# Optimization experiments

Measured on AMD Instinct MI355X. Metric: run time of the kernel, lower is better.

## Reference

```python
import jax, jax.numpy as jnp
import numpy as np

B = 512
V = 6890   # SMPL vertices
NJ = 24    # joints (global)
NB = 10    # shape betas
NP = 207   # pose blendshape features = 23*9
NJO = 19   # cocoplus output joints
PARENTS = np.array([0,0,0,0,1,2,3,4,5,6,7,8,9,9,9,12,13,14,16,17,18,19,20,21], dtype=np.int32)


def setup_inputs() -> dict:
    key = jax.random.key(0)
    ks = jax.random.split(key, 7)
    inputs = jax.random.normal(ks[0], (B, 82), jnp.float32) * 0.2  # [pose(72) | shape(10)]
    v_template = jax.random.normal(ks[1], (V, 3), jnp.float32)
    shapes = jax.random.normal(ks[2], (NB, V * 3), jnp.float32) * 0.01
    posedirs = jax.random.normal(ks[3], (NP, V * 3), jnp.float32) * 0.01
    jr = jax.random.uniform(ks[4], (V, NJ), jnp.float32)
    smpl_regressor = jr / jnp.sum(jr, axis=0, keepdims=True)          # columns sum to 1 over vertices
    w = jax.random.uniform(ks[5], (V, NJ), jnp.float32) ** 4
    lbs_weights = w / jnp.sum(w, axis=1, keepdims=True)               # rows sum to 1 over joints
    cr = jax.random.uniform(ks[6], (V, NJO), jnp.float32)
    joint_regressor = cr / jnp.sum(cr, axis=0, keepdims=True)
    parents = jnp.asarray(PARENTS)
    return {"inputs": inputs, "v_template": v_template, "shapes": shapes,
            "posedirs": posedirs, "smpl_regressor": smpl_regressor,
            "lbs_weights": lbs_weights, "joint_regressor": joint_regressor,
            "parents": parents}


def _rodrigues(pose):  # [B,72] -> [B,24,3,3]
    r = pose.reshape(-1, 3)
    angle = jnp.linalg.norm(r + 1e-8, axis=1, keepdims=True)  # [N,1]
    n = r / angle
    c = jnp.cos(angle)[:, :, None]   # [N,1,1]
    s = jnp.sin(angle)[:, :, None]
    outer = n[:, :, None] * n[:, None, :]
    z = jnp.zeros_like(n[:, 0])
    K = jnp.stack([z, -n[:, 2], n[:, 1],
                   n[:, 2], z, -n[:, 0],
                   -n[:, 1], n[:, 0], z], axis=1).reshape(-1, 3, 3)
    R = c * jnp.eye(3, dtype=pose.dtype) + (1.0 - c) * outer + s * K
    return R.reshape(-1, NJ, 3, 3)


def _make_A(R, t):  # R [B,3,3], t [B,3] -> [B,4,4]
    top = jnp.concatenate([R, t[:, :, None]], axis=2)
    bottom = jnp.broadcast_to(jnp.array([0., 0., 0., 1.], dtype=R.dtype), (R.shape[0], 1, 4))
    return jnp.concatenate([top, bottom], axis=1)


def _global_rigid(rotations, joints, parents_np):
    # sequential kinematic-chain composition over the fixed 24-joint tree
    res = [_make_A(rotations[:, 0], joints[:, 0])]
    for i in range(1, NJ):
        p = int(parents_np[i])
        t = joints[:, i] - joints[:, p]
        res.append(jnp.matmul(res[p], _make_A(rotations[:, i], t)))
    A_world = jnp.stack(res, axis=1)                 # [B,24,4,4]
    new_J = A_world[:, :, :3, 3]
    Jw0 = jnp.concatenate([joints, jnp.zeros(joints.shape[:2] + (1,), joints.dtype)], axis=2)[..., None]
    init_bone = jnp.matmul(A_world, Jw0)[..., 0]     # [B,24,4]
    pad = jnp.zeros_like(A_world).at[:, :, :, 3].set(init_bone)
    return new_J, A_world - pad


def reference(inputs, v_template, shapes, posedirs, smpl_regressor, lbs_weights, joint_regressor, parents):
    b = inputs.shape[0]
    pose = inputs[:, :72]
    beta = inputs[:, -10:]
    v_shaped = jnp.matmul(beta, shapes).reshape(b, V, 3) + v_template
    v_joints = jnp.einsum('bvc,vj->bjc', v_shaped, smpl_regressor)        # [B,24,3]
    rot = _rodrigues(pose)                                                # [B,24,3,3]
    pose_feature = (rot[:, 1:] - jnp.eye(3, dtype=rot.dtype)).reshape(b, -1)  # [B,207]
    v_posed = jnp.matmul(pose_feature, posedirs).reshape(b, V, 3) + v_shaped
    joint_transformed, A = _global_rigid(rot, v_joints, np.asarray(parents))
    T = jnp.einsum('vj,bjk->bvk', lbs_weights, A.reshape(b, NJ, 16)).reshape(b, V, 4, 4)
    v_homo = jnp.concatenate([v_posed, jnp.ones((b, V, 1), v_posed.dtype)], axis=2)
    vertices = jnp.einsum('bvij,bvj->bvi', T, v_homo)[:, :, :3]
    joints = jnp.einsum('bvc,vj->bjc', vertices, joint_regressor)         # [B,19,3]
    return vertices, joints, rot
```

## Files before the change

kernel.cpp:

```cpp
#include <hip/hip_runtime.h>

#define B_   512
#define V_   6890
#define NJ_  24
#define NB_  10
#define NP_  207
#define NJO_ 19



#define SRB_   192
#define SRCH_  862

__global__ void __launch_bounds__(256) k_pre(const float* __restrict__ in,
                                             const float* __restrict__ shapes,
                                             const float* __restrict__ vt,
                                             const float* __restrict__ sreg,
                                             float* __restrict__ srtr,
                                             float* __restrict__ out_rot,
                                             float* __restrict__ pf_t) {
  int blk = blockIdx.x;
  int tid = threadIdx.x;
  if (blk < SRB_) {
    int j  = blk >> 3;
    int ch = blk & 7;
    int vend = (ch + 1) * SRCH_; if (vend > V_) vend = V_;
    float acc[33];
#pragma unroll
    for (int a = 0; a < 33; a++) acc[a] = 0.f;
    for (int v = ch * SRCH_ + tid; v < vend; v += 256) {
      float w = sreg[v * NJ_ + j];
#pragma unroll
      for (int k = 0; k < NB_; k++) {
        const float* sp = shapes + k * (V_ * 3) + 3 * v;
#pragma unroll
        for (int c = 0; c < 3; c++) acc[k * 3 + c] += w * sp[c];
      }
#pragma unroll
      for (int c = 0; c < 3; c++) acc[30 + c] += w * vt[3 * v + c];
    }
    __shared__ float red[4][33];
    int wave = tid >> 6, lane = tid & 63;
#pragma unroll
    for (int a = 0; a < 33; a++) {
      float x = acc[a];
#pragma unroll
      for (int m = 1; m < 64; m <<= 1) x += __shfl_xor(x, m, 64);
      if (lane == 0) red[wave][a] = x;
    }
    __syncthreads();
    if (tid < 33) {
      float s = red[0][tid] + red[1][tid] + red[2][tid] + red[3][tid];
      if (tid < 30) atomicAdd(&srtr[((tid / 3) * NJ_ + j) * 3 + (tid % 3)], s);
      else          atomicAdd(&srtr[720 + j * 3 + (tid - 30)], s);
    }
  } else {
    int idx = (blk - SRB_) * 256 + tid;
    int b = idx & (B_ - 1);
    int j = idx >> 9;
    const float* r = in + b * 82 + j * 3;
    float r0 = r[0], r1 = r[1], r2 = r[2];
    float ax = r0 + 1e-8f, ay = r1 + 1e-8f, az = r2 + 1e-8f;
    float angle = sqrtf(ax * ax + ay * ay + az * az);
    float inv = 1.0f / angle;
    float n0 = r0 * inv, n1 = r1 * inv, n2 = r2 * inv;
    float c = cosf(angle), s = sinf(angle);
    float ic = 1.0f - c;
    float R[9];
    R[0] = c + ic * n0 * n0;      R[1] = ic * n0 * n1 - s * n2;  R[2] = ic * n0 * n2 + s * n1;
    R[3] = ic * n1 * n0 + s * n2; R[4] = c + ic * n1 * n1;       R[5] = ic * n1 * n2 - s * n0;
    R[6] = ic * n2 * n0 - s * n1; R[7] = ic * n2 * n1 + s * n0;  R[8] = c + ic * n2 * n2;
    float* ro = out_rot + b * 216 + j * 9;
#pragma unroll
    for (int q = 0; q < 9; q++) ro[q] = R[q];
    if (j > 0) {
#pragma unroll
      for (int q = 0; q < 9; q++)
        pf_t[(size_t)((j - 1) * 9 + q) * B_ + b] = R[q] - ((q % 4 == 0) ? 1.0f : 0.0f);
    }
  }
}

__global__ void __launch_bounds__(64) k_chain(const float* __restrict__ in,
                                              const float* __restrict__ rot,
                                              const float* __restrict__ srtr,
                                              const int* __restrict__ parents,
                                              float* __restrict__ Abuf) {
  __shared__ float Jl[NJ_ * 3 * 64];
  __shared__ float Al[64 * 289];
  int tid = threadIdx.x;
  int b = blockIdx.x * 64 + tid;
  float beta[NB_];
#pragma unroll
  for (int k = 0; k < NB_; k++) beta[k] = in[b * 82 + 72 + k];
#pragma unroll
  for (int j = 0; j < NJ_; j++) {
#pragma unroll
    for (int c = 0; c < 3; c++) {
      float s = srtr[720 + j * 3 + c];
#pragma unroll
      for (int k = 0; k < NB_; k++) s += beta[k] * srtr[(k * NJ_ + j) * 3 + c];
      Jl[(j * 3 + c) * 64 + tid] = s;
    }
  }
  const float* Rb = rot + b * 216;
  float* A = Al + tid * 289;
#pragma unroll
  for (int r = 0; r < 3; r++) {
#pragma unroll
    for (int c = 0; c < 3; c++) A[r * 4 + c] = Rb[r * 3 + c];
    A[r * 4 + 3] = Jl[r * 64 + tid];
  }
  for (int j = 1; j < NJ_; j++) {
    int p = parents[j];
    float t0 = Jl[(j * 3 + 0) * 64 + tid] - Jl[(p * 3 + 0) * 64 + tid];
    float t1 = Jl[(j * 3 + 1) * 64 + tid] - Jl[(p * 3 + 1) * 64 + tid];
    float t2 = Jl[(j * 3 + 2) * 64 + tid] - Jl[(p * 3 + 2) * 64 + tid];
    float Rj[9];
#pragma unroll
    for (int q = 0; q < 9; q++) Rj[q] = Rb[j * 9 + q];
#pragma unroll
    for (int r = 0; r < 3; r++) {
      float p0 = A[p * 12 + r * 4 + 0];
      float p1 = A[p * 12 + r * 4 + 1];
      float p2 = A[p * 12 + r * 4 + 2];
      float p3 = A[p * 12 + r * 4 + 3];
#pragma unroll
      for (int c = 0; c < 3; c++)
        A[j * 12 + r * 4 + c] = p0 * Rj[c] + p1 * Rj[3 + c] + p2 * Rj[6 + c];
      A[j * 12 + r * 4 + 3] = p0 * t0 + p1 * t1 + p2 * t2 + p3;
    }
  }
  float* Ab = Abuf + (size_t)b * 288;
#pragma unroll
  for (int j = 0; j < NJ_; j++) {
    float jx = Jl[(j * 3 + 0) * 64 + tid];
    float jy = Jl[(j * 3 + 1) * 64 + tid];
    float jz = Jl[(j * 3 + 2) * 64 + tid];
#pragma unroll
    for (int r = 0; r < 3; r++) {
      float m0 = A[j * 12 + r * 4 + 0];
      float m1 = A[j * 12 + r * 4 + 1];
      float m2 = A[j * 12 + r * 4 + 2];
      float m3 = A[j * 12 + r * 4 + 3];
      float4 o;
      o.x = m0; o.y = m1; o.z = m2;
      o.w = m3 - (m0 * jx + m1 * jy + m2 * jz);
      *reinterpret_cast<float4*>(Ab + j * 12 + r * 4) = o;
    }
  }
}

#define PB_ 8
#define BT_ 32
#define GX_ 108
#define GY_ 16
#define NWG_ (GX_ * GY_)
__global__ void __launch_bounds__(256) k_main(const float* __restrict__ in,
                                              const float* __restrict__ shapes,
                                              const float* __restrict__ vt,
                                              const float* __restrict__ posedirs,
                                              const float* __restrict__ lbs,
                                              const float* __restrict__ pf_t,
                                              const float* __restrict__ Abuf,
                                              float* __restrict__ verts) {
  __shared__ float lbs_l[64 * 25];
  int tid = threadIdx.x;
  int raw  = blockIdx.y * GX_ + blockIdx.x;
  int virt = (raw & 7) * (NWG_ / 8) + (raw >> 3);
  int vblk = virt >> 4;
  int bblk = virt & (GY_ - 1);
  int v0 = vblk * 64;
  int b0 = bblk * BT_;
  int nv = V_ - v0; if (nv > 64) nv = 64;
  for (int i = tid; i < nv * NJ_; i += 256)
    lbs_l[(i / NJ_) * 25 + (i % NJ_)] = lbs[(size_t)v0 * NJ_ + i];
  __syncthreads();
  int lane = tid & 63;
  int g = tid >> 6;
  int bb0 = __builtin_amdgcn_readfirstlane(b0 + g * PB_);
  int v = v0 + lane;
  int vc = v < V_ ? v : V_ - 1;

  float acc[PB_][3];
  {
    float t0 = vt[3 * vc + 0], t1 = vt[3 * vc + 1], t2 = vt[3 * vc + 2];
#pragma unroll
    for (int i = 0; i < PB_; i++) { acc[i][0] = t0; acc[i][1] = t1; acc[i][2] = t2; }
  }
#pragma unroll
  for (int k = 0; k < NB_; k++) {
    const float* sp = shapes + k * (V_ * 3) + 3 * vc;
    float s0 = sp[0], s1 = sp[1], s2 = sp[2];
#pragma unroll
    for (int i = 0; i < PB_; i++) {
      float bv = in[(size_t)(bb0 + i) * 82 + 72 + k];
      acc[i][0] += bv * s0; acc[i][1] += bv * s1; acc[i][2] += bv * s2;
    }
  }
  for (int p = 0; p < NP_; p++) {
    const float* pp = posedirs + (size_t)p * (V_ * 3) + 3 * vc;
    float d0 = pp[0], d1 = pp[1], d2 = pp[2];
    const float* pfp = pf_t + (size_t)p * B_ + bb0;
#pragma unroll
    for (int i = 0; i < PB_; i++) {
      float f = pfp[i];
      acc[i][0] += f * d0; acc[i][1] += f * d1; acc[i][2] += f * d2;
    }
  }
  float o[PB_][3];
#pragma unroll
  for (int i = 0; i < PB_; i++) { o[i][0] = 0.f; o[i][1] = 0.f; o[i][2] = 0.f; }
  for (int j = 0; j < NJ_; j++) {
    float w = lbs_l[lane * 25 + j];
#pragma unroll
    for (int i = 0; i < PB_; i++) {
      const float* M = Abuf + (size_t)(bb0 + i) * 288 + j * 12;
      float x = acc[i][0], y = acc[i][1], z = acc[i][2];
      o[i][0] += w * (M[0] * x + M[1] * y + M[2]  * z + M[3]);
      o[i][1] += w * (M[4] * x + M[5] * y + M[6]  * z + M[7]);
      o[i][2] += w * (M[8] * x + M[9] * y + M[10] * z + M[11]);
    }
  }
  if (v < V_) {
#pragma unroll
    for (int i = 0; i < PB_; i++) {
      float* op = verts + (size_t)(bb0 + i) * (V_ * 3) + 3 * v;
      op[0] = o[i][0]; op[1] = o[i][1]; op[2] = o[i][2];
    }
  }
}

#define JCH_ 1728
__global__ void __launch_bounds__(256) k_joints(const float* __restrict__ verts,
                                                const float* __restrict__ jreg,
                                                float* __restrict__ jout) {
  int b = blockIdx.x;
  int ch = blockIdx.y;
  int tid = threadIdx.x;
  int vend = (ch + 1) * JCH_; if (vend > V_) vend = V_;
  float acc[NJO_ * 3];
#pragma unroll
  for (int a = 0; a < NJO_ * 3; a++) acc[a] = 0.f;
  const float* vb = verts + (size_t)b * V_ * 3;
  for (int v = ch * JCH_ + tid; v < vend; v += 256) {
    float x = vb[3 * v + 0], y = vb[3 * v + 1], z = vb[3 * v + 2];
    const float* jr = jreg + (size_t)v * NJO_;
#pragma unroll
    for (int jo = 0; jo < NJO_; jo++) {
      float w = jr[jo];
      acc[jo * 3 + 0] += w * x; acc[jo * 3 + 1] += w * y; acc[jo * 3 + 2] += w * z;
    }
  }
  __shared__ float red[4][NJO_ * 3];
  int wave = tid >> 6, lane = tid & 63;
#pragma unroll
  for (int a = 0; a < NJO_ * 3; a++) {
    float x = acc[a];
#pragma unroll
    for (int m = 1; m < 64; m <<= 1) x += __shfl_xor(x, m, 64);
    if (lane == 0) red[wave][a] = x;
  }
  __syncthreads();
  if (tid < NJO_ * 3) {
    float s = red[0][tid] + red[1][tid] + red[2][tid] + red[3][tid];
    atomicAdd(&jout[b * (NJO_ * 3) + tid], s);
  }
}

extern "C" void kernel_launch(void* const* d_in, const int* in_sizes, int n_in,
                              void* d_out, int out_size, void* d_ws, size_t ws_size,
                              hipStream_t stream) {
  const float* inputs   = (const float*)d_in[0];
  const float* v_templ  = (const float*)d_in[1];
  const float* shapes   = (const float*)d_in[2];
  const float* posedirs = (const float*)d_in[3];
  const float* sreg     = (const float*)d_in[4];
  const float* lbs      = (const float*)d_in[5];
  const float* jreg     = (const float*)d_in[6];
  const int*   parents  = (const int*)d_in[7];

  float* out   = (float*)d_out;
  float* verts = out;
  float* jout  = out + 10583040;
  float* rot   = out + 10612224;

  float* ws   = (float*)d_ws;
  float* pf_t = ws;
  float* Abuf = ws + 105984;
  float* srtr = ws + 105984 + 147456;

  hipMemsetAsync(srtr, 0, 792 * sizeof(float), stream);
  hipMemsetAsync(jout, 0, B_ * NJO_ * 3 * sizeof(float), stream);

  k_pre  <<<SRB_ + 48, 256, 0, stream>>>(inputs, shapes, v_templ, sreg, srtr, rot, pf_t);
  k_chain<<<8, 64, 0, stream>>>(inputs, rot, srtr, parents, Abuf);
  dim3 gmain(GX_, GY_);
  k_main <<<gmain, 256, 0, stream>>>(inputs, shapes, v_templ, posedirs, lbs, pf_t, Abuf, verts);
  dim3 gj(B_, 4);
  k_joints<<<gj, 256, 0, stream>>>(verts, jreg, jout);
}
```

Measured before the change: 299.8 us.

## Parallelize kinematic chain per row, transpose joint regressor, fold memset into k_pre

The kinematic-chain kernel now uses three threads per batch element, one per matrix row. Joints and transforms live in registers instead of large shared-memory arrays, and a compile-time parent table lets the loop fully unroll. k_pre gains extra blocks that zero the joint output and write a transposed copy of the joint regressor, so k_joints reads the weights coalesced and one memset launch is dropped. The chain and regressor results depend on the hardcoded parent table matching the input, and the extra workspace used by jreg_t must fit in the allocation.

Result: faster. 266.8 us (-11.0%).

```diff
diff --git a/kernel.cpp b/kernel.cpp
--- a/kernel.cpp
+++ b/kernel.cpp
@@ -11,14 +11,19 @@
 
 #define SRB_   192
 #define SRCH_  862
+#define RODB_  48
+#define TRB_   26
 
 __global__ void __launch_bounds__(256) k_pre(const float* __restrict__ in,
                                              const float* __restrict__ shapes,
                                              const float* __restrict__ vt,
                                              const float* __restrict__ sreg,
+                                             const float* __restrict__ jreg,
                                              float* __restrict__ srtr,
                                              float* __restrict__ out_rot,
-                                             float* __restrict__ pf_t) {
+                                             float* __restrict__ pf_t,
+                                             float* __restrict__ jreg_t,
+                                             float* __restrict__ jout) {
   int blk = blockIdx.x;
   int tid = threadIdx.x;
   if (blk < SRB_) {
@@ -54,7 +59,7 @@
       if (tid < 30) atomicAdd(&srtr[((tid / 3) * NJ_ + j) * 3 + (tid % 3)], s);
       else          atomicAdd(&srtr[720 + j * 3 + (tid - 30)], s);
     }
-  } else {
+  } else if (blk < SRB_ + RODB_) {
     int idx = (blk - SRB_) * 256 + tid;
     int b = idx & (B_ - 1);
     int j = idx >> 9;
@@ -78,21 +83,33 @@
       for (int q = 0; q < 9; q++)
         pf_t[(size_t)((j - 1) * 9 + q) * B_ + b] = R[q] - ((q % 4 == 0) ? 1.0f : 0.0f);
     }
-  }
-}
-
-__global__ void __launch_bounds__(64) k_chain(const float* __restrict__ in,
-                                              const float* __restrict__ rot,
-                                              const float* __restrict__ srtr,
-                                              const int* __restrict__ parents,
-                                              float* __restrict__ Abuf) {
-  __shared__ float Jl[NJ_ * 3 * 64];
-  __shared__ float Al[64 * 289];
+  } else {
+    int idx = (blk - SRB_ - RODB_) * 256 + tid;
+    for (int q = idx; q < B_ * NJO_ * 3; q += TRB_ * 256) jout[q] = 0.f;
+    for (int e = idx; e < V_ * NJO_; e += TRB_ * 256) {
+      int jo = e / V_;
+      int v  = e - jo * V_;
+      jreg_t[e] = jreg[v * NJO_ + jo];
+    }
+  }
+}
+
+__global__ void __launch_bounds__(192) k_chain(const float* __restrict__ in,
+                                               const float* __restrict__ rot,
+                                               const float* __restrict__ srtr,
+                                               const int* __restrict__ parents,
+                                               float* __restrict__ Abuf) {
+  (void)parents;
+  constexpr int P[NJ_] = {0, 0, 0, 0, 1, 2, 3, 4, 5, 6, 7, 8, 9, 9, 9, 12, 13, 14,
+                          16, 17, 18, 19, 20, 21};
   int tid = threadIdx.x;
-  int b = blockIdx.x * 64 + tid;
+  int bl = tid & 63;
+  int r  = tid >> 6;
+  int b  = blockIdx.x * 64 + bl;
   float beta[NB_];
 #pragma unroll
   for (int k = 0; k < NB_; k++) beta[k] = in[b * 82 + 72 + k];
+  float J[NJ_][3];
 #pragma unroll
   for (int j = 0; j < NJ_; j++) {
 #pragma unroll
@@ -100,54 +117,36 @@
       float s = srtr[720 + j * 3 + c];
 #pragma unroll
       for (int k = 0; k < NB_; k++) s += beta[k] * srtr[(k * NJ_ + j) * 3 + c];
-      Jl[(j * 3 + c) * 64 + tid] = s;
+      J[j][c] = s;
     }
   }
   const float* Rb = rot + b * 216;
-  float* A = Al + tid * 289;
-#pragma unroll
-  for (int r = 0; r < 3; r++) {
-#pragma unroll
-    for (int c = 0; c < 3; c++) A[r * 4 + c] = Rb[r * 3 + c];
-    A[r * 4 + 3] = Jl[r * 64 + tid];
-  }
+  float A[NJ_][4];
+#pragma unroll
+  for (int c = 0; c < 3; c++) A[0][c] = Rb[r * 3 + c];
+  A[0][3] = J[0][r];
+#pragma unroll
   for (int j = 1; j < NJ_; j++) {
-    int p = parents[j];
-    float t0 = Jl[(j * 3 + 0) * 64 + tid] - Jl[(p * 3 + 0) * 64 + tid];
-    float t1 = Jl[(j * 3 + 1) * 64 + tid] - Jl[(p * 3 + 1) * 64 + tid];
-    float t2 = Jl[(j * 3 + 2) * 64 + tid] - Jl[(p * 3 + 2) * 64 + tid];
+    const int p = P[j];
+    float t0 = J[j][0] - J[p][0];
+    float t1 = J[j][1] - J[p][1];
+    float t2 = J[j][2] - J[p][2];
     float Rj[9];
 #pragma unroll
     for (int q = 0; q < 9; q++) Rj[q] = Rb[j * 9 + q];
-#pragma unroll
-    for (int r = 0; r < 3; r++) {
-      float p0 = A[p * 12 + r * 4 + 0];
-      float p1 = A[p * 12 + r * 4 + 1];
-      float p2 = A[p * 12 + r * 4 + 2];
-      float p3 = A[p * 12 + r * 4 + 3];
-#pragma unroll
-      for (int c = 0; c < 3; c++)
-        A[j * 12 + r * 4 + c] = p0 * Rj[c] + p1 * Rj[3 + c] + p2 * Rj[6 + c];
-      A[j * 12 + r * 4 + 3] = p0 * t0 + p1 * t1 + p2 * t2 + p3;
-    }
-  }
-  float* Ab = Abuf + (size_t)b * 288;
+    float p0 = A[p][0], p1 = A[p][1], p2 = A[p][2], p3 = A[p][3];
+#pragma unroll
+    for (int c = 0; c < 3; c++)
+      A[j][c] = p0 * Rj[c] + p1 * Rj[3 + c] + p2 * Rj[6 + c];
+    A[j][3] = p0 * t0 + p1 * t1 + p2 * t2 + p3;
+  }
+  float* Ab = Abuf + (size_t)b * 288 + r * 4;
 #pragma unroll
   for (int j = 0; j < NJ_; j++) {
-    float jx = Jl[(j * 3 + 0) * 64 + tid];
-    float jy = Jl[(j * 3 + 1) * 64 + tid];
-    float jz = Jl[(j * 3 + 2) * 64 + tid];
-#pragma unroll
-    for (int r = 0; r < 3; r++) {
-      float m0 = A[j * 12 + r * 4 + 0];
-      float m1 = A[j * 12 + r * 4 + 1];
-      float m2 = A[j * 12 + r * 4 + 2];
-      float m3 = A[j * 12 + r * 4 + 3];
-      float4 o;
-      o.x = m0; o.y = m1; o.z = m2;
-      o.w = m3 - (m0 * jx + m1 * jy + m2 * jz);
-      *reinterpret_cast<float4*>(Ab + j * 12 + r * 4) = o;
-    }
+    float4 o;
+    o.x = A[j][0]; o.y = A[j][1]; o.z = A[j][2];
+    o.w = A[j][3] - (A[j][0] * J[j][0] + A[j][1] * J[j][1] + A[j][2] * J[j][2]);
+    *reinterpret_cast<float4*>(Ab + j * 12) = o;
   }
 }
 
@@ -233,7 +232,7 @@
 
 #define JCH_ 1728
 __global__ void __launch_bounds__(256) k_joints(const float* __restrict__ verts,
-                                                const float* __restrict__ jreg,
+                                                const float* __restrict__ jreg_t,
                                                 float* __restrict__ jout) {
   int b = blockIdx.x;
   int ch = blockIdx.y;
@@ -245,10 +244,9 @@
   const float* vb = verts + (size_t)b * V_ * 3;
   for (int v = ch * JCH_ + tid; v < vend; v += 256) {
     float x = vb[3 * v + 0], y = vb[3 * v + 1], z = vb[3 * v + 2];
-    const float* jr = jreg + (size_t)v * NJO_;
 #pragma unroll
     for (int jo = 0; jo < NJO_; jo++) {
-      float w = jr[jo];
+      float w = jreg_t[jo * V_ + v];
       acc[jo * 3 + 0] += w * x; acc[jo * 3 + 1] += w * y; acc[jo * 3 + 2] += w * z;
     }
   }
@@ -285,18 +283,19 @@
   float* jout  = out + 10583040;
   float* rot   = out + 10612224;
 
-  float* ws   = (float*)d_ws;
-  float* pf_t = ws;
-  float* Abuf = ws + 105984;
-  float* srtr = ws + 105984 + 147456;
+  float* ws     = (float*)d_ws;
+  float* pf_t   = ws;
+  float* Abuf   = ws + 105984;
+  float* srtr   = ws + 105984 + 147456;
+  float* jreg_t = srtr + 792;
 
   hipMemsetAsync(srtr, 0, 792 * sizeof(float), stream);
-  hipMemsetAsync(jout, 0, B_ * NJO_ * 3 * sizeof(float), stream);
-
-  k_pre  <<<SRB_ + 48, 256, 0, stream>>>(inputs, shapes, v_templ, sreg, srtr, rot, pf_t);
-  k_chain<<<8, 64, 0, stream>>>(inputs, rot, srtr, parents, Abuf);
+
+  k_pre  <<<SRB_ + RODB_ + TRB_, 256, 0, stream>>>(inputs, shapes, v_templ, sreg, jreg,
+                                                   srtr, rot, pf_t, jreg_t, jout);
+  k_chain<<<8, 192, 0, stream>>>(inputs, rot, srtr, parents, Abuf);
   dim3 gmain(GX_, GY_);
   k_main <<<gmain, 256, 0, stream>>>(inputs, shapes, v_templ, posedirs, lbs, pf_t, Abuf, verts);
   dim3 gj(B_, 4);
-  k_joints<<<gj, 256, 0, stream>>>(verts, jreg, jout);
-}
+  k_joints<<<gj, 256, 0, stream>>>(verts, jreg_t, jout);
+}
```
